# Optimization experiments

Hardware: AMD Instinct MI355X
Metric: run time of the kernel (lower is better)

## Reference

```python
import jax, jax.numpy as jnp
import numpy as np

N = 1048576        # batch
DTOT = 64          # total dims in u
D = 32             # transformed dims (len(nodes))
K = 40             # knots = num spline bins
B = 5.0            # tail bound: bins/2 = ceil(max|limit|)


def setup_inputs() -> dict:
    key = jax.random.key(0)
    k1, k2, k3, k4 = jax.random.split(key, 4)
    # scale inputs so they cover many bins and some fall in the identity tails
    u = jax.random.normal(k1, (N, DTOT), jnp.float32) * 3.0
    w = jax.random.uniform(k2, (D, K), jnp.float32, -0.5, 0.5)
    h = jax.random.uniform(k3, (D, K), jnp.float32, -0.5, 0.5)
    d = jax.random.uniform(k4, (D, K - 1), jnp.float32, -0.5, 0.5)
    nodes = jnp.arange(D, dtype=jnp.int32)
    return {"u": u, "w": w, "h": h, "d": d, "nodes": nodes}


def _rqs_forward(x, w, h, d):
    # x: [N, D] selected dims; w,h: [D, K]; d: [D, K-1]
    dt = x.dtype
    widths = jax.nn.softmax(w, axis=-1) * (2.0 * B)          # [D, K]
    cumw = jnp.concatenate(
        [jnp.full((D, 1), -B, dt), -B + jnp.cumsum(widths, -1)], -1)  # [D, K+1]
    heights = jax.nn.softmax(h, axis=-1) * (2.0 * B)
    cumh = jnp.concatenate(
        [jnp.full((D, 1), -B, dt), -B + jnp.cumsum(heights, -1)], -1)
    # interior derivatives via softplus, boundary derivatives fixed to 1 (linear tails)
    derivs = jnp.concatenate(
        [jnp.ones((D, 1), dt), jax.nn.softplus(d), jnp.ones((D, 1), dt)], -1)  # [D, K+1]

    inside = jnp.abs(x) <= B
    xc = jnp.clip(x, -B, B)
    # per-dim bin search (irregular, data-dependent)
    idx = jax.vmap(lambda kn, xd: jnp.searchsorted(kn, xd, side='right'))(cumw, xc.T).T - 1
    idx = jnp.clip(idx, 0, K - 1)                             # [N, D]

    dd = jnp.arange(D)[None, :]
    cw = cumw[dd, idx]; bw = widths[dd, idx]
    ch = cumh[dd, idx]; bh = heights[dd, idx]
    d0 = derivs[dd, idx]; d1 = derivs[dd, idx + 1]
    delta = bh / bw                                            # bin slope

    theta = (xc - cw) / bw
    t1m = theta * (1.0 - theta)
    denom = delta + (d0 + d1 - 2.0 * delta) * t1m
    num = bh * (delta * theta * theta + d0 * t1m)
    y = ch + num / denom
    logdet = (jnp.log(delta * delta * (d1 * theta * theta
                                       + 2.0 * delta * t1m
                                       + d0 * (1.0 - theta) ** 2))
              - 2.0 * jnp.log(denom))

    y = jnp.where(inside, y, x)                # identity tails
    logdet = jnp.where(inside, logdet, 0.0)
    return y, logdet.sum(-1)                   # [N, D], [N]


def reference(u, w, h, d, nodes):
    y, logd = _rqs_forward(u[:, nodes], w, h, d)
    x = u.at[:, nodes].set(y)
    return x, logd
```

## Files before the change

kernel.cpp:

```cpp
#include <hip/hip_runtime.h>
#include <math.h>

#define NROWS 1048576
#define DTOT  64
#define D     32
#define K     40
#define Bf    5.0f
#define G     256

#define OFF_CUMW 0
#define OFF_DER  (D*(K+1))
#define OFF_T1   (2*D*(K+1))
#define OFF_GS_BYTES ((2*D*(K+1) + 4*D*K) * 4)
#define WS_BYTES (OFF_GS_BYTES + D*G)

__global__ __launch_bounds__(64) void build_tables(
    const float* __restrict__ w, const float* __restrict__ h,
    const float* __restrict__ dk,
    float* __restrict__ cumw_g, float* __restrict__ der_g,
    float4* __restrict__ T1_g, unsigned char* __restrict__ gs_g)
{
    const int j = blockIdx.x;
    const int k = threadIdx.x;
    __shared__ float s_cumw[K + 1];

    float wv = (k < K) ? w[j * K + k] : -INFINITY;
    float hv = (k < K) ? h[j * K + k] : -INFINITY;
    float mw = wv, mh = hv;
    for (int m = 32; m > 0; m >>= 1) {
        mw = fmaxf(mw, __shfl_xor(mw, m));
        mh = fmaxf(mh, __shfl_xor(mh, m));
    }
    float ew = (k < K) ? __expf(wv - mw) : 0.f;
    float eh = (k < K) ? __expf(hv - mh) : 0.f;
    float sw = ew, sh = eh;
    for (int m = 32; m > 0; m >>= 1) {
        sw += __shfl_xor(sw, m);
        sh += __shfl_xor(sh, m);
    }
    float width  = ew / sw * (2.f * Bf);
    float height = eh / sh * (2.f * Bf);

    float iw = width, ih = height;
    for (int off = 1; off < 64; off <<= 1) {
        float a = __shfl_up(iw, off);
        float b = __shfl_up(ih, off);
        if (k >= off) { iw += a; ih += b; }
    }
    float cw_k = -Bf + (iw - width);
    float ch_k = -Bf + (ih - height);

    if (k <= K) {
        float dv = 1.f;
        if (k > 0 && k < K) dv = log1pf(__expf(dk[j * (K - 1) + (k - 1)]));
        der_g[j * (K + 1) + k] = dv;
    }
    if (k < K) {
        cumw_g[j * (K + 1) + k] = cw_k;
        s_cumw[k] = cw_k;
        T1_g[j * K + k] = make_float4(cw_k, 1.f / width, ch_k, height);
    }
    if (k == K - 1) {
        cumw_g[j * (K + 1) + K] = -Bf + iw;
        s_cumw[K] = -Bf + iw;
    }
    __syncthreads();

    for (int c = k; c < G; c += 64) {
        float L = -Bf + (2.f * Bf) * ((float)c / (float)G);
        int idx = 0;
        for (int m = 1; m < K; ++m)
            if (s_cumw[m] <= L) idx = m;
        gs_g[j * G + c] = (unsigned char)idx;
    }
}

__global__ __launch_bounds__(256) void rqs_main(
    const float4* __restrict__ u4,
    const float* __restrict__ cumw_g, const float* __restrict__ der_g,
    const float4* __restrict__ T1_g, const unsigned char* __restrict__ gs_g,
    float4* __restrict__ x4, float* __restrict__ logd, int ntiles)
{
    __shared__ float  s_cumw[D * (K + 1)];
    __shared__ float  s_der [D * (K + 1)];
    __shared__ float4 s_T1  [D * K];
    __shared__ unsigned char s_gs[D * G];

    const int t = threadIdx.x;
    for (int i = t; i < D * (K + 1); i += 256) {
        s_cumw[i] = cumw_g[i];
        s_der[i]  = der_g[i];
    }
    for (int i = t; i < D * K; i += 256) s_T1[i] = T1_g[i];
    for (int i = t; i < D * G / 16; i += 256)
        ((uint4*)s_gs)[i] = ((const uint4*)gs_g)[i];
    __syncthreads();

    const int seg = t & 15;
    const int grp = t >> 4;

    for (int tile = blockIdx.x; tile < ntiles; tile += gridDim.x) {
        const int row = tile * 16 + grp;
        float4 v = u4[row * 16 + seg];
        float ld = 0.f;

        if (seg < 8) {
            float vv[4] = {v.x, v.y, v.z, v.w};
#pragma unroll
            for (int c = 0; c < 4; ++c) {
                const int j = seg * 4 + c;
                const float x = vv[c];
                const bool inside = fabsf(x) <= Bf;
                const float xc = fminf(fmaxf(x, -Bf), Bf);

                int cell = (int)((xc + Bf) * (G / (2.f * Bf)));
                cell = min(cell, G - 1);
                int i = s_gs[j * G + cell];
                const float* cwrow = s_cumw + j * (K + 1);
                while (i < K - 1 && cwrow[i + 1] <= xc) ++i;

                const float4 tt = s_T1[j * K + i];
                const float cw = tt.x, rbw = tt.y, ch = tt.z, bh = tt.w;
                const float d0 = s_der[j * (K + 1) + i];
                const float d1 = s_der[j * (K + 1) + i + 1];

                const float delta = bh * rbw;
                const float theta = (xc - cw) * rbw;
                const float omt   = 1.f - theta;
                const float t1m   = theta * omt;
                const float th2   = theta * theta;
                const float denom = fmaf(fmaf(-2.f, delta, d0 + d1), t1m, delta);
                const float num   = bh * fmaf(d0, t1m, delta * th2);
                const float rd    = __builtin_amdgcn_rcpf(denom);
                const float y     = fmaf(num, rd, ch);
                const float Ap    = fmaf(d1, th2,
                                     fmaf(2.f * delta, t1m, d0 * omt * omt));
                const float ldet  = __logf(delta * delta * Ap * rd * rd);

                vv[c] = inside ? y : x;
                ld += inside ? ldet : 0.f;
            }
            v = make_float4(vv[0], vv[1], vv[2], vv[3]);
        }
        x4[row * 16 + seg] = v;

        ld += __shfl_xor(ld, 1);
        ld += __shfl_xor(ld, 2);
        ld += __shfl_xor(ld, 4);
        ld += __shfl_xor(ld, 8);
        if (seg == 0) logd[row] = ld;
    }
}

extern "C" void kernel_launch(void* const* d_in, const int* in_sizes, int n_in,
                              void* d_out, int out_size, void* d_ws, size_t ws_size,
                              hipStream_t stream) {
    const float* u  = (const float*)d_in[0];
    const float* w  = (const float*)d_in[1];
    const float* h  = (const float*)d_in[2];
    const float* dk = (const float*)d_in[3];

    float* ws    = (float*)d_ws;
    float* cumw  = ws + OFF_CUMW;
    float* der   = ws + OFF_DER;
    float4* T1   = (float4*)((char*)d_ws + OFF_T1 * 4);
    unsigned char* gs = (unsigned char*)d_ws + OFF_GS_BYTES;

    float* xout = (float*)d_out;
    float* logd = (float*)d_out + (size_t)NROWS * DTOT;

    build_tables<<<D, 64, 0, stream>>>(w, h, dk, cumw, der, T1, gs);

    const int ntiles = NROWS / 16;
    rqs_main<<<1024, 256, 0, stream>>>((const float4*)u, cumw, der, T1, gs,
                                       (float4*)xout, logd, ntiles);
}
```

Baseline: 481.4 us.

## Shrink LDS tables and give every thread a transformed segment

The separate cumulative-width table is dropped, and the bin walk now tests theta>=1 using the packed float4 table instead. The grid lookup is halved to 128 cells with padded rows, which cuts LDS use and lets 5 blocks fit per CU. Each thread now handles one transformed float4 and also copies one passthrough float4, so no lanes sit idle on the untouched dims. A coarser grid means more linear-walk steps per lookup, and the theta-based walk may differ slightly at bin edges.

```diff
diff --git a/kernel.cpp b/kernel.cpp
--- a/kernel.cpp
+++ b/kernel.cpp
@@ -6,19 +6,20 @@
 #define D     32
 #define K     40
 #define Bf    5.0f
-#define G     256
+#define G     128
+#define GS    132
+#define TP    (K + 1)
 
-#define OFF_CUMW 0
-#define OFF_DER  (D*(K+1))
-#define OFF_T1   (2*D*(K+1))
-#define OFF_GS_BYTES ((2*D*(K+1) + 4*D*K) * 4)
-#define WS_BYTES (OFF_GS_BYTES + D*G)
+#define OFF_T1   0
+#define OFF_DER  (D * TP * 16)
+#define OFF_GS   (OFF_DER + D * TP * 4)
+#define WS_BYTES (OFF_GS + D * G)
 
 __global__ __launch_bounds__(64) void build_tables(
     const float* __restrict__ w, const float* __restrict__ h,
     const float* __restrict__ dk,
-    float* __restrict__ cumw_g, float* __restrict__ der_g,
-    float4* __restrict__ T1_g, unsigned char* __restrict__ gs_g)
+    float* __restrict__ der_g, float4* __restrict__ T1_g,
+    unsigned char* __restrict__ gs_g)
 {
     const int j = blockIdx.x;
     const int k = threadIdx.x;
@@ -53,17 +54,15 @@
     if (k <= K) {
         float dv = 1.f;
         if (k > 0 && k < K) dv = log1pf(__expf(dk[j * (K - 1) + (k - 1)]));
-        der_g[j * (K + 1) + k] = dv;
+        der_g[j * TP + k] = dv;
     }
     if (k < K) {
-        cumw_g[j * (K + 1) + k] = cw_k;
         s_cumw[k] = cw_k;
-        T1_g[j * K + k] = make_float4(cw_k, 1.f / width, ch_k, height);
+        T1_g[j * TP + k] = make_float4(cw_k, 1.f / width, ch_k, height);
     }
-    if (k == K - 1) {
-        cumw_g[j * (K + 1) + K] = -Bf + iw;
-        s_cumw[K] = -Bf + iw;
-    }
+    if (k == K - 1) s_cumw[K] = -Bf + iw;
+    if (k == K) T1_g[j * TP + K] = make_float4(0.f, 0.f, 0.f, 0.f);
+
     __syncthreads();
 
     for (int c = k; c < G; c += 64) {
@@ -75,79 +74,80 @@
     }
 }
 
-__global__ __launch_bounds__(256) void rqs_main(
+__global__ __launch_bounds__(256, 5) void rqs_main(
     const float4* __restrict__ u4,
-    const float* __restrict__ cumw_g, const float* __restrict__ der_g,
-    const float4* __restrict__ T1_g, const unsigned char* __restrict__ gs_g,
+    const float* __restrict__ der_g, const float4* __restrict__ T1_g,
+    const unsigned char* __restrict__ gs_g,
     float4* __restrict__ x4, float* __restrict__ logd, int ntiles)
 {
-    __shared__ float  s_cumw[D * (K + 1)];
-    __shared__ float  s_der [D * (K + 1)];
-    __shared__ float4 s_T1  [D * K];
-    __shared__ unsigned char s_gs[D * G];
+    __shared__ float4 s_T1[D * TP];
+    __shared__ float  s_der[D * TP];
+    __shared__ unsigned char s_gs[D * GS];
 
     const int t = threadIdx.x;
-    for (int i = t; i < D * (K + 1); i += 256) {
-        s_cumw[i] = cumw_g[i];
-        s_der[i]  = der_g[i];
+    for (int i = t; i < D * TP; i += 256) {
+        s_T1[i]  = T1_g[i];
+        s_der[i] = der_g[i];
     }
-    for (int i = t; i < D * K; i += 256) s_T1[i] = T1_g[i];
-    for (int i = t; i < D * G / 16; i += 256)
-        ((uint4*)s_gs)[i] = ((const uint4*)gs_g)[i];
+    for (int i = t; i < D * G; i += 256)
+        s_gs[(i >> 7) * GS + (i & (G - 1))] = gs_g[i];
     __syncthreads();
 
-    const int seg = t & 15;
-    const int grp = t >> 4;
+    const int seg = t & 7;
+    const int rl  = t >> 3;
 
     for (int tile = blockIdx.x; tile < ntiles; tile += gridDim.x) {
-        const int row = tile * 16 + grp;
-        float4 v = u4[row * 16 + seg];
+        const int row = tile * 32 + rl;
+
+        const float4 vp = u4[row * 16 + 8 + seg];
+        float4 v        = u4[row * 16 + seg];
+        x4[row * 16 + 8 + seg] = vp;
+
+        float vv[4] = {v.x, v.y, v.z, v.w};
         float ld = 0.f;
+#pragma unroll
+        for (int c = 0; c < 4; ++c) {
+            const int j = seg * 4 + c;
+            const float x = vv[c];
+            const bool inside = fabsf(x) <= Bf;
+            const float xc = fminf(fmaxf(x, -Bf), Bf);
 
-        if (seg < 8) {
-            float vv[4] = {v.x, v.y, v.z, v.w};
-#pragma unroll
-            for (int c = 0; c < 4; ++c) {
-                const int j = seg * 4 + c;
-                const float x = vv[c];
-                const bool inside = fabsf(x) <= Bf;
-                const float xc = fminf(fmaxf(x, -Bf), Bf);
+            int cell = (int)((xc + Bf) * (G / (2.f * Bf)));
+            cell = min(cell, G - 1);
+            int i = s_gs[j * GS + cell];
 
-                int cell = (int)((xc + Bf) * (G / (2.f * Bf)));
-                cell = min(cell, G - 1);
-                int i = s_gs[j * G + cell];
-                const float* cwrow = s_cumw + j * (K + 1);
-                while (i < K - 1 && cwrow[i + 1] <= xc) ++i;
+            float4 tt = s_T1[j * TP + i];
+            float theta = (xc - tt.x) * tt.y;
+            while (theta >= 1.f && i < K - 1) {
+                ++i;
+                tt = s_T1[j * TP + i];
+                theta = (xc - tt.x) * tt.y;
+            }
 
-                const float4 tt = s_T1[j * K + i];
-                const float cw = tt.x, rbw = tt.y, ch = tt.z, bh = tt.w;
-                const float d0 = s_der[j * (K + 1) + i];
-                const float d1 = s_der[j * (K + 1) + i + 1];
+            const float rbw = tt.y, ch = tt.z, bh = tt.w;
+            const float d0 = s_der[j * TP + i];
+            const float d1 = s_der[j * TP + i + 1];
 
-                const float delta = bh * rbw;
-                const float theta = (xc - cw) * rbw;
-                const float omt   = 1.f - theta;
-                const float t1m   = theta * omt;
-                const float th2   = theta * theta;
-                const float denom = fmaf(fmaf(-2.f, delta, d0 + d1), t1m, delta);
-                const float num   = bh * fmaf(d0, t1m, delta * th2);
-                const float rd    = __builtin_amdgcn_rcpf(denom);
-                const float y     = fmaf(num, rd, ch);
-                const float Ap    = fmaf(d1, th2,
-                                     fmaf(2.f * delta, t1m, d0 * omt * omt));
-                const float ldet  = __logf(delta * delta * Ap * rd * rd);
+            const float delta = bh * rbw;
+            const float omt   = 1.f - theta;
+            const float t1m   = theta * omt;
+            const float th2   = theta * theta;
+            const float denom = fmaf(fmaf(-2.f, delta, d0 + d1), t1m, delta);
+            const float num   = bh * fmaf(d0, t1m, delta * th2);
+            const float rd    = __builtin_amdgcn_rcpf(denom);
+            const float y     = fmaf(num, rd, ch);
+            const float Ap    = fmaf(d1, th2,
+                                 fmaf(2.f * delta, t1m, d0 * omt * omt));
+            const float ldet  = __logf(delta * delta * Ap * rd * rd);
 
-                vv[c] = inside ? y : x;
-                ld += inside ? ldet : 0.f;
-            }
-            v = make_float4(vv[0], vv[1], vv[2], vv[3]);
+            vv[c] = inside ? y : x;
+            ld += inside ? ldet : 0.f;
         }
-        x4[row * 16 + seg] = v;
+        x4[row * 16 + seg] = make_float4(vv[0], vv[1], vv[2], vv[3]);
 
         ld += __shfl_xor(ld, 1);
         ld += __shfl_xor(ld, 2);
         ld += __shfl_xor(ld, 4);
-        ld += __shfl_xor(ld, 8);
         if (seg == 0) logd[row] = ld;
     }
 }
@@ -160,18 +160,16 @@
     const float* h  = (const float*)d_in[2];
     const float* dk = (const float*)d_in[3];
 
-    float* ws    = (float*)d_ws;
-    float* cumw  = ws + OFF_CUMW;
-    float* der   = ws + OFF_DER;
-    float4* T1   = (float4*)((char*)d_ws + OFF_T1 * 4);
-    unsigned char* gs = (unsigned char*)d_ws + OFF_GS_BYTES;
+    float4* T1        = (float4*)d_ws;
+    float*  der       = (float*)((char*)d_ws + OFF_DER);
+    unsigned char* gs = (unsigned char*)d_ws + OFF_GS;
 
     float* xout = (float*)d_out;
     float* logd = (float*)d_out + (size_t)NROWS * DTOT;
 
-    build_tables<<<D, 64, 0, stream>>>(w, h, dk, cumw, der, T1, gs);
+    build_tables<<<D, 64, 0, stream>>>(w, h, dk, der, T1, gs);
 
-    const int ntiles = NROWS / 16;
-    rqs_main<<<1024, 256, 0, stream>>>((const float4*)u, cumw, der, T1, gs,
+    const int ntiles = NROWS / 32;
+    rqs_main<<<1280, 256, 0, stream>>>((const float4*)u, der, T1, gs,
                                        (float4*)xout, logd, ntiles);
 }
```

New measurement: 454.3 us. 1.06x faster.
